# Performance work log

Hardware: AMD Instinct MI355X
Metric: run time of the kernel (lower is better)

Reference implementation:

```python
import jax, jax.numpy as jnp
import numpy as np

N_NODES = 33
EPS = 1e-5


def _tconv(x, w, b):
    # x: (B,T,N,Ci); w: (3,O,Ci,1,ks); b: (3,O). Gated temporal conv: relu(P*sigmoid(Q)+R)
    xt = jnp.transpose(x, (0, 3, 2, 1))  # (B,Ci,N,T)
    def c(i):
        y = jax.lax.conv_general_dilated(xt, w[i], (1, 1), 'VALID',
                                         dimension_numbers=('NCHW', 'OIHW', 'NCHW'))
        return y + b[i][None, :, None, None]
    P, Q, R = c(0), c(1), c(2)
    H = jax.nn.relu(P * jax.nn.sigmoid(Q) + R)
    return jnp.transpose(H, (0, 3, 2, 1))  # (B,T',N,O)


def _cheb(x, edge_index, Wk, bias):
    # ChebConv K=3, sym normalization, lambda_max=2 => L_hat = -D^{-1/2} A D^{-1/2} (diag cancels)
    src, tgt = edge_index[0], edge_index[1]
    w = jnp.ones((src.shape[0],), x.dtype)
    deg = jnp.zeros((N_NODES,), x.dtype).at[src].add(w)
    dinv = jnp.where(deg > 0, deg ** -0.5, 0.0)
    lap_w = -dinv[src] * w * dinv[tgt]

    def prop(z):  # z: (B,T,N,C); sparse matvec over edges, aggregate at target
        zg = z[:, :, src, :] * lap_w[None, None, :, None]
        return jnp.zeros_like(z).at[:, :, tgt, :].add(zg)

    Tx0 = x
    Tx1 = prop(Tx0)
    Tx2 = 2.0 * prop(Tx1) - Tx0
    out = (jnp.einsum('btnc,cd->btnd', Tx0, Wk[0])
           + jnp.einsum('btnc,cd->btnd', Tx1, Wk[1])
           + jnp.einsum('btnc,cd->btnd', Tx2, Wk[2]))
    return out + bias


def _bn(x, g, b):
    # BatchNorm2d(num_nodes): stats per node over (B,T,C); biased variance, train-mode stats
    mean = x.mean(axis=(0, 1, 3), keepdims=True)
    var = x.var(axis=(0, 1, 3), keepdims=True)
    return (x - mean) * jax.lax.rsqrt(var + EPS) * g[None, None, :, None] + b[None, None, :, None]


def _stconv(x, ei, tc1w, tc1b, cw, cb, tc2w, tc2b, bng, bnb):
    t = _tconv(x, tc1w, tc1b)
    t = jax.nn.relu(_cheb(t, ei, cw, cb))
    t = _tconv(t, tc2w, tc2b)
    return _bn(t, bng, bnb)


def setup_inputs() -> dict:
    key = jax.random.key(0)
    ks = jax.random.split(key, 24)
    s = 0.05
    inp = {
        'x': jax.random.normal(ks[0], (32, 512, 33, 3), jnp.float32),
        'edge_index': jax.random.randint(ks[1], (2, 64), 0, 33, jnp.int64) if jax.config.jax_enable_x64 else jax.random.randint(ks[1], (2, 64), 0, 33).astype(jnp.int32),
        # STConv 1 (in=3, hid=out=64)
        's1_tc1_w': jax.random.normal(ks[2], (3, 64, 3, 1, 3), jnp.float32) * s,
        's1_tc1_b': jax.random.normal(ks[3], (3, 64), jnp.float32) * s,
        's1_cheb_w': jax.random.normal(ks[4], (3, 64, 64), jnp.float32) * s,
        's1_cheb_b': jax.random.normal(ks[5], (64,), jnp.float32) * s,
        's1_tc2_w': jax.random.normal(ks[6], (3, 64, 64, 1, 3), jnp.float32) * s,
        's1_tc2_b': jax.random.normal(ks[7], (3, 64), jnp.float32) * s,
        's1_bn_g': jnp.ones((33,), jnp.float32),
        's1_bn_b': jnp.zeros((33,), jnp.float32),
        # STConv 2 (in=64, hid=out=64)
        's2_tc1_w': jax.random.normal(ks[8], (3, 64, 64, 1, 3), jnp.float32) * s,
        's2_tc1_b': jax.random.normal(ks[9], (3, 64), jnp.float32) * s,
        's2_cheb_w': jax.random.normal(ks[10], (3, 64, 64), jnp.float32) * s,
        's2_cheb_b': jax.random.normal(ks[11], (64,), jnp.float32) * s,
        's2_tc2_w': jax.random.normal(ks[12], (3, 64, 64, 1, 3), jnp.float32) * s,
        's2_tc2_b': jax.random.normal(ks[13], (3, 64), jnp.float32) * s,
        's2_bn_g': jnp.ones((33,), jnp.float32),
        's2_bn_b': jnp.zeros((33,), jnp.float32),
        # classifier: Linear(64*33 -> 256), Linear(256 -> 10)
        'fc1_w': jax.random.normal(ks[14], (64 * 33, 256), jnp.float32) * s,
        'fc1_b': jax.random.normal(ks[15], (256,), jnp.float32) * s,
        'fc2_w': jax.random.normal(ks[16], (256, 10), jnp.float32) * s,
        'fc2_b': jax.random.normal(ks[17], (10,), jnp.float32) * s,
    }
    return inp


def reference(x, edge_index,
              s1_tc1_w, s1_tc1_b, s1_cheb_w, s1_cheb_b, s1_tc2_w, s1_tc2_b, s1_bn_g, s1_bn_b,
              s2_tc1_w, s2_tc1_b, s2_cheb_w, s2_cheb_b, s2_tc2_w, s2_tc2_b, s2_bn_g, s2_bn_b,
              fc1_w, fc1_b, fc2_w, fc2_b):
    h = jax.nn.relu(_stconv(x, edge_index, s1_tc1_w, s1_tc1_b, s1_cheb_w, s1_cheb_b,
                            s1_tc2_w, s1_tc2_b, s1_bn_g, s1_bn_b))
    h = jax.nn.relu(_stconv(h, edge_index, s2_tc1_w, s2_tc1_b, s2_cheb_w, s2_cheb_b,
                            s2_tc2_w, s2_tc2_b, s2_bn_g, s2_bn_b))
    h = h.mean(axis=1)                      # (B, N, C) mean over time
    h = h.reshape(h.shape[0], -1)           # (B, N*C)
    h = jax.nn.relu(h @ fc1_w + fc1_b)      # dropout = identity (eval)
    return h @ fc2_w + fc2_b                # (B, num_classes)
```

## Files before the change

### kernel.cpp

```cpp
#include <hip/hip_runtime.h>
#include <math.h>

#define NN 33
#define NC 2112

typedef __attribute__((ext_vector_type(8))) short bfrag;
typedef __attribute__((ext_vector_type(4))) float f32x4;

#define OFF_LT   0
#define OFF_L2T  2244
#define OFF_UP1  4488
#define OFF_UP2  16776
#define OFF_WT0  29064
#define OFF_WT1  65928
#define OFF_WT2  102792
#define OFF_ST1  139656
#define OFF_ST2  139722
#define OFF_HB   139856
#define OFF_MEAN 148048
#define OFF_A    215632
#define A_ELEMS  34332672ull
#define SLAB     1077120ull

__device__ inline unsigned short f2bf(float x) {
  unsigned int u = __float_as_uint(x);
  unsigned int r = (u + 0x7fffu + ((u >> 16) & 1u)) >> 16;
  return (unsigned short)r;
}
__device__ inline float bf2f(unsigned short h) {
  return __uint_as_float(((unsigned int)h) << 16);
}

__global__ __launch_bounds__(256) void k_prep_lap(
    const int* __restrict__ ei, float* __restrict__ ws) {
  __shared__ float Lsm[1089];
  __shared__ float L2sm[1089];
  __shared__ float deg[NN];
  __shared__ float dinv[NN];
  int tid = threadIdx.x;
  for (int i = tid; i < 1089; i += 256) Lsm[i] = 0.f;
  if (tid < NN) deg[tid] = 0.f;
  __syncthreads();
  if (tid < 64) atomicAdd(&deg[ei[tid]], 1.f);
  __syncthreads();
  if (tid < NN) dinv[tid] = deg[tid] > 0.f ? rsqrtf(deg[tid]) : 0.f;
  __syncthreads();
  if (tid < 64) {
    int s = ei[tid], t = ei[64 + tid];
    atomicAdd(&Lsm[t * NN + s], -dinv[s] * dinv[t]);
  }
  __syncthreads();
  for (int i = tid; i < 1089; i += 256) {
    int r = i / NN, c = i % NN;
    float s = 0.f;
    for (int m = 0; m < NN; m++) s += Lsm[r * NN + m] * Lsm[m * NN + c];
    L2sm[i] = 2.f * s;
  }
  __syncthreads();
  for (int i = tid; i < 33 * 66; i += 256) {
    int m = i / 66, nn = i % 66;
    int n33 = nn < 33 ? nn : nn - 33;
    ws[OFF_LT + m * 68 + nn]  = Lsm[n33 * NN + m];
    ws[OFF_L2T + m * 68 + nn] = L2sm[n33 * NN + m];
  }
}

__global__ __launch_bounds__(256) void k_prep_w(
    const float* __restrict__ cw1, const float* __restrict__ cw2,
    const float* __restrict__ tw0, const float* __restrict__ tw1,
    const float* __restrict__ tw2, float* __restrict__ ws) {
  int u = blockIdx.x * 256 + threadIdx.x;
  if (u < 24576) {
    unsigned short* u1 = (unsigned short*)(ws + OFF_UP1);
    unsigned short* u2 = (unsigned short*)(ws + OFF_UP2);
    int j = u & 7;
    int nn = (u >> 3) & 15;
    int q = (u >> 7) & 3;
    int sp = (u >> 9) & 1;
    int blk = u >> 10;
    int nt = blk & 3;
    int ks = blk >> 2;
    int k = ks * 32 + q * 8 + j;
    int d = nt * 16 + nn;
    int s = k >> 6, cc = k & 63;
    float v1 = cw1[(s * 64 + cc) * 64 + d];
    float v2 = cw2[(s * 64 + cc) * 64 + d];
    if (s == 0) { v1 -= cw1[(128 + cc) * 64 + d]; v2 -= cw2[(128 + cc) * 64 + d]; }
    unsigned short h1 = f2bf(v1);
    u1[u] = sp ? f2bf(v1 - bf2f(h1)) : h1;
    unsigned short h2 = f2bf(v2);
    u2[u] = sp ? f2bf(v2 - bf2f(h2)) : h2;
  }
  {
    unsigned short* p0 = (unsigned short*)(ws + OFF_WT0);
    unsigned short* p1 = (unsigned short*)(ws + OFF_WT1);
    unsigned short* p2 = (unsigned short*)(ws + OFF_WT2);
    int j  = u & 7;
    int nn_ = (u >> 3) & 15;
    int q  = (u >> 7) & 3;
    int B  = u >> 9;
    int sp = B & 1;
    int B2 = B >> 1;
    int nt = B2 % 12;
    int dk = B2 / 12;
    int ks = dk & 1;
    int dt = dk >> 1;
    int o  = nt * 16 + nn_;
    int ci = ks * 32 + q * 8 + j;
    int src = (o * 64 + ci) * 3 + dt;
    float w0 = tw0[src], w1 = tw1[src], w2 = tw2[src];
    unsigned short h;
    h = f2bf(w0); p0[u] = sp ? f2bf(w0 - bf2f(h)) : h;
    h = f2bf(w1); p1[u] = sp ? f2bf(w1 - bf2f(h)) : h;
    h = f2bf(w2); p2[u] = sp ? f2bf(w2 - bf2f(h)) : h;
  }
}

__global__ __launch_bounds__(256) void k_tconv0(
    const float* __restrict__ x, const float* __restrict__ w,
    const float* __restrict__ bias, float* __restrict__ out,
    int b0, int total) {
  __shared__ float wsm[1728];
  __shared__ float bsm[192];
  int tid = threadIdx.x;
  for (int i = tid; i < 1728; i += 256) wsm[i] = w[i];
  if (tid < 192) bsm[tid] = bias[tid];
  __syncthreads();
  int idx = blockIdx.x * 256 + tid;
  if (idx >= total) return;
  int ch = idx & 63;
  int r = idx >> 6;
  int n = r % NN; r /= NN;
  int t = r % 510;
  int bc = r / 510;
  int b = b0 + bc;
  float aP = bsm[ch], aQ = bsm[64 + ch], aR = bsm[128 + ch];
  const float* xp = x + ((size_t)(b * 512 + t) * NN + n) * 3;
  #pragma unroll
  for (int dt = 0; dt < 3; dt++) {
    float x0 = xp[dt * 99 + 0], x1 = xp[dt * 99 + 1], x2 = xp[dt * 99 + 2];
    aP += x0 * wsm[(ch * 3 + 0) * 3 + dt] + x1 * wsm[(ch * 3 + 1) * 3 + dt] + x2 * wsm[(ch * 3 + 2) * 3 + dt];
    aQ += x0 * wsm[((64 + ch) * 3 + 0) * 3 + dt] + x1 * wsm[((64 + ch) * 3 + 1) * 3 + dt] + x2 * wsm[((64 + ch) * 3 + 2) * 3 + dt];
    aR += x0 * wsm[((128 + ch) * 3 + 0) * 3 + dt] + x1 * wsm[((128 + ch) * 3 + 1) * 3 + dt] + x2 * wsm[((128 + ch) * 3 + 2) * 3 + dt];
  }
  float sg = 1.f / (1.f + __expf(-aQ));
  out[(size_t)(bc * 510 + t) * NC + n * 64 + ch] = fmaxf(aP * sg + aR, 0.f);
}

__global__ __launch_bounds__(256, 4) void k_chebmm(
    const float* __restrict__ in, const unsigned short* __restrict__ Uf,
    const float* __restrict__ cbias, float* __restrict__ out,
    const float* __restrict__ ws, int totalRows) {
  __shared__ __attribute__((aligned(16))) unsigned short Zh[64 * 136];
  __shared__ __attribute__((aligned(16))) unsigned short Zl[64 * 136];

  int tid = threadIdx.x;
  int R0 = blockIdx.x * 64;
  int c = tid & 63;
  int g = __builtin_amdgcn_readfirstlane(tid >> 6);
  int Rg = R0 + g * 16;
  int btg = Rg / 33;
  int n0 = Rg - btg * 33;
  int wrap = 33 - n0;

  const float* lt  = ws + OFF_LT;
  const float* l2t = ws + OFF_L2T;
  const float* ipA = in + (size_t)btg * NC + c;
  const float* ipB = ipA + NC;
  float z1[16], z2[16];
  #pragma unroll
  for (int rr = 0; rr < 16; rr++) { z1[rr] = 0.f; z2[rr] = 0.f; }
  #pragma unroll 3
  for (int m = 0; m < NN; m++) {
    float hvA = ipA[m * 64];
    float hvB = ipB[m * 64];
    const float* ltm  = lt + m * 68 + n0;
    const float* l2tm = l2t + m * 68 + n0;
    #pragma unroll
    for (int rr = 0; rr < 16; rr++) {
      float hv = (rr < wrap) ? hvA : hvB;
      z1[rr] += ltm[rr] * hv;
      z2[rr] += l2tm[rr] * hv;
    }
  }
  #pragma unroll
  for (int rr = 0; rr < 16; rr++) {
    int r = g * 16 + rr;
    unsigned short zh1 = f2bf(z1[rr]);
    Zh[r * 136 + c] = zh1;
    Zl[r * 136 + c] = f2bf(z1[rr] - bf2f(zh1));
    unsigned short zh2 = f2bf(z2[rr]);
    Zh[r * 136 + 64 + c] = zh2;
    Zl[r * 136 + 64 + c] = f2bf(z2[rr] - bf2f(zh2));
  }

  int lane = tid & 63;
  int m15 = lane & 15, q = lane >> 4;
  f32x4 acc[4];
  #pragma unroll
  for (int nt = 0; nt < 4; nt++) acc[nt] = (f32x4){0.f, 0.f, 0.f, 0.f};

  const float* hrow = in + (size_t)(Rg + m15) * 64 + q * 8;
  float hv0[8], hv1[8];
  *(float4*)&hv0[0] = *(const float4*)(hrow);
  *(float4*)&hv0[4] = *(const float4*)(hrow + 4);
  *(float4*)&hv1[0] = *(const float4*)(hrow + 32);
  *(float4*)&hv1[4] = *(const float4*)(hrow + 36);

  bfrag uh[4], ul[4];
  #pragma unroll
  for (int nt = 0; nt < 4; nt++) {
    const unsigned short* bp = Uf + nt * 1024 + lane * 8;
    uh[nt] = *(const bfrag*)bp;
    ul[nt] = *(const bfrag*)(bp + 512);
  }

  #pragma unroll
  for (int ks = 0; ks < 6; ks++) {
    bfrag nh[4], nl[4];
    if (ks < 5) {
      #pragma unroll
      for (int nt = 0; nt < 4; nt++) {
        const unsigned short* bp = Uf + ((ks + 1) * 4 + nt) * 1024 + lane * 8;
        nh[nt] = *(const bfrag*)bp;
        nl[nt] = *(const bfrag*)(bp + 512);
      }
    }
    bfrag ah, al;
    if (ks < 2) {
      const float* hv = (ks == 0) ? hv0 : hv1;
      union { bfrag v; unsigned short s[8]; } Ahf, Alf;
      #pragma unroll
      for (int j = 0; j < 8; j++) {
        unsigned short hh = f2bf(hv[j]);
        Ahf.s[j] = hh;
        Alf.s[j] = f2bf(hv[j] - bf2f(hh));
      }
      ah = Ahf.v; al = Alf.v;
    } else {
      int aoff = (g * 16 + m15) * 136 + (ks - 2) * 32 + q * 8;
      ah = *(const bfrag*)(Zh + aoff);
      al = *(const bfrag*)(Zl + aoff);
    }
    #pragma unroll
    for (int nt = 0; nt < 4; nt++) {
      acc[nt] = __builtin_amdgcn_mfma_f32_16x16x32_bf16(ah, uh[nt], acc[nt], 0, 0, 0);
      acc[nt] = __builtin_amdgcn_mfma_f32_16x16x32_bf16(ah, ul[nt], acc[nt], 0, 0, 0);
      acc[nt] = __builtin_amdgcn_mfma_f32_16x16x32_bf16(al, uh[nt], acc[nt], 0, 0, 0);
    }
    #pragma unroll
    for (int nt = 0; nt < 4; nt++) { uh[nt] = nh[nt]; ul[nt] = nl[nt]; }
  }
  #pragma unroll
  for (int nt = 0; nt < 4; nt++) {
    int d = nt * 16 + m15;
    float bd = cbias[d];
    #pragma unroll
    for (int rr = 0; rr < 4; rr++) {
      int R = R0 + g * 16 + q * 4 + rr;
      if (R < totalRows)
        out[(size_t)R * 64 + d] = fmaxf(acc[nt][rr] + bd, 0.f);
    }
  }
}

__global__ __launch_bounds__(256, 4) void k_tconv(
    const float* __restrict__ in, int inStride, int Tin,
    const unsigned short* __restrict__ wsp, const float* __restrict__ bias,
    float* __restrict__ out, int outStride, int Tout,
    const float* __restrict__ bnSt, const float* __restrict__ bnG,
    const float* __restrict__ bnB, float bnCnt, float* __restrict__ statsOut) {
  __shared__ __attribute__((aligned(16))) unsigned short Ah[66 * 72];
  __shared__ __attribute__((aligned(16))) unsigned short Al[66 * 72];
  __shared__ float red[8];
  int tid = threadIdx.x;
  int ntt = (Tout + 63) >> 6;
  int tpb = NN * ntt;
  int bc = blockIdx.x / tpb, r = blockIdx.x % tpb;
  int n = r / ntt, tt = r % ntt;
  int t0 = tt << 6;
  const float* ip = in + (size_t)bc * inStride * NC + n * 64;

  float sc = 1.f, sh = 0.f;
  if (bnSt) {
    float mean = bnSt[n] / bnCnt;
    float var = bnSt[33 + n] / bnCnt - mean * mean;
    sc = rsqrtf(var + 1e-5f) * bnG[n];
    sh = bnB[n] - mean * sc;
  }
  for (int i = tid; i < 66 * 16; i += 256) {
    int row = i >> 4, c4 = i & 15;
    float4 v = make_float4(0.f, 0.f, 0.f, 0.f);
    if (t0 + row < Tin) v = *(const float4*)(ip + (size_t)(t0 + row) * NC + c4 * 4);
    if (bnSt) {
      v.x = fmaxf(v.x * sc + sh, 0.f);
      v.y = fmaxf(v.y * sc + sh, 0.f);
      v.z = fmaxf(v.z * sc + sh, 0.f);
      v.w = fmaxf(v.w * sc + sh, 0.f);
    }
    unsigned short h0 = f2bf(v.x), h1 = f2bf(v.y), h2 = f2bf(v.z), h3 = f2bf(v.w);
    unsigned short l0 = f2bf(v.x - bf2f(h0)), l1 = f2bf(v.y - bf2f(h1));
    unsigned short l2 = f2bf(v.z - bf2f(h2)), l3 = f2bf(v.w - bf2f(h3));
    uint2 ph, pl;
    ph.x = (unsigned)h0 | ((unsigned)h1 << 16); ph.y = (unsigned)h2 | ((unsigned)h3 << 16);
    pl.x = (unsigned)l0 | ((unsigned)l1 << 16); pl.y = (unsigned)l2 | ((unsigned)l3 << 16);
    *(uint2*)(Ah + row * 72 + c4 * 4) = ph;
    *(uint2*)(Al + row * 72 + c4 * 4) = pl;
  }
  __syncthreads();

  int lane = tid & 63;
  int wv = tid >> 6;
  int m15 = lane & 15, q = lane >> 4;

  f32x4 acc[4][3];
  #pragma unroll
  for (int mi = 0; mi < 4; mi++)
    #pragma unroll
    for (int j = 0; j < 3; j++) acc[mi][j] = (f32x4){0.f, 0.f, 0.f, 0.f};

  #pragma unroll
  for (int s = 0; s < 6; s++) {
    int dt = s >> 1, ks = s & 1;
    const unsigned short* wdt = wsp + (size_t)dt * 24576;
    bfrag bh[3], bl[3];
    #pragma unroll
    for (int j = 0; j < 3; j++) {
      int nt = wv + 4 * j;
      const unsigned short* bp = wdt + ((ks * 12 + nt) * 2) * 512 + lane * 8;
      bh[j] = *(const bfrag*)bp;
      bl[j] = *(const bfrag*)(bp + 512);
    }
    bfrag ah[4], al[4];
    #pragma unroll
    for (int mi = 0; mi < 4; mi++) {
      int row = mi * 16 + m15 + dt;
      int off = row * 72 + ks * 32 + q * 8;
      ah[mi] = *(const bfrag*)(Ah + off);
      al[mi] = *(const bfrag*)(Al + off);
    }
    #pragma unroll
    for (int j = 0; j < 3; j++)
      #pragma unroll
      for (int mi = 0; mi < 4; mi++) {
        acc[mi][j] = __builtin_amdgcn_mfma_f32_16x16x32_bf16(ah[mi], bh[j], acc[mi][j], 0, 0, 0);
        acc[mi][j] = __builtin_amdgcn_mfma_f32_16x16x32_bf16(ah[mi], bl[j], acc[mi][j], 0, 0, 0);
        acc[mi][j] = __builtin_amdgcn_mfma_f32_16x16x32_bf16(al[mi], bh[j], acc[mi][j], 0, 0, 0);
      }
  }

  float ssum = 0.f, sq = 0.f;
  int ch = wv * 16 + m15;
  float bP = bias[ch], bQ = bias[64 + ch], bR = bias[128 + ch];
  #pragma unroll
  for (int mi = 0; mi < 4; mi++) {
    #pragma unroll
    for (int rr = 0; rr < 4; rr++) {
      int t = t0 + mi * 16 + q * 4 + rr;
      float P = acc[mi][0][rr] + bP;
      float Q = acc[mi][1][rr] + bQ;
      float Rv = acc[mi][2][rr] + bR;
      float sg = 1.f / (1.f + __expf(-Q));
      float h = fmaxf(P * sg + Rv, 0.f);
      if (t < Tout) {
        out[(size_t)(bc * outStride + t) * NC + n * 64 + ch] = h;
        ssum += h; sq += h * h;
      }
    }
  }
  if (statsOut) {
    #pragma unroll
    for (int d = 32; d > 0; d >>= 1) {
      ssum += __shfl_down(ssum, d);
      sq += __shfl_down(sq, d);
    }
    if (lane == 0) { red[wv] = ssum; red[4 + wv] = sq; }
    __syncthreads();
    if (tid == 0) {
      atomicAdd(&statsOut[n], red[0] + red[1] + red[2] + red[3]);
      atomicAdd(&statsOut[33 + n], red[4] + red[5] + red[6] + red[7]);
    }
  }
}

__global__ __launch_bounds__(256) void k_bnmean(
    const float* __restrict__ A, int stride, int Tv,
    const float* __restrict__ st, const float* __restrict__ gg,
    const float* __restrict__ bb, float* __restrict__ mout) {
  int idx = blockIdx.x * 256 + threadIdx.x;
  int p = idx % NC, b = idx / NC;
  int n = p >> 6;
  float cnt = (float)(32 * Tv * 64);
  float mean = st[n] / cnt;
  float var = st[33 + n] / cnt - mean * mean;
  float sc = rsqrtf(var + 1e-5f) * gg[n];
  float sh = bb[n] - mean * sc;
  float acc = 0.f;
  const float* ap = A + (size_t)b * stride * NC + p;
  for (int t = 0; t < Tv; t += 4) {
    acc += fmaxf(ap[(size_t)t * NC] * sc + sh, 0.f)
         + fmaxf(ap[(size_t)(t + 1) * NC] * sc + sh, 0.f)
         + fmaxf(ap[(size_t)(t + 2) * NC] * sc + sh, 0.f)
         + fmaxf(ap[(size_t)(t + 3) * NC] * sc + sh, 0.f);
  }
  mout[idx] = acc / (float)Tv;
}

__global__ __launch_bounds__(256) void k_fc1(
    const float* __restrict__ meanb, const float* __restrict__ w1,
    float* __restrict__ hb) {
  int b = blockIdx.x >> 3, ks = blockIdx.x & 7;
  int d = threadIdx.x;
  const float* mp = meanb + b * NC + ks * 264;
  const float* wp = w1 + (size_t)(ks * 264) * 256 + d;
  float acc = 0.f;
  for (int k = 0; k < 264; k += 8) {
    #pragma unroll
    for (int u = 0; u < 8; u++)
      acc += mp[k + u] * wp[(size_t)(k + u) * 256];
  }
  atomicAdd(&hb[b * 256 + d], acc);
}

__global__ __launch_bounds__(256) void k_fc2(
    const float* __restrict__ hb, const float* __restrict__ b1,
    const float* __restrict__ w2, const float* __restrict__ b2,
    float* __restrict__ out) {
  __shared__ float h[256];
  int tid = threadIdx.x, b = blockIdx.x;
  h[tid] = fmaxf(hb[b * 256 + tid] + b1[tid], 0.f);
  __syncthreads();
  if (tid < 10) {
    float a = b2[tid];
    for (int k = 0; k < 256; k++) a += h[k] * w2[k * 10 + tid];
    out[b * 10 + tid] = a;
  }
}

extern "C" void kernel_launch(void* const* d_in, const int* in_sizes, int n_in,
                              void* d_out, int out_size, void* d_ws, size_t ws_size,
                              hipStream_t stream) {
  const float* x        = (const float*)d_in[0];
  const int*   ei       = (const int*)d_in[1];
  const float* s1_tc1_w = (const float*)d_in[2];
  const float* s1_tc1_b = (const float*)d_in[3];
  const float* s1_cheb_w= (const float*)d_in[4];
  const float* s1_cheb_b= (const float*)d_in[5];
  const float* s1_tc2_w = (const float*)d_in[6];
  const float* s1_tc2_b = (const float*)d_in[7];
  const float* s1_bn_g  = (const float*)d_in[8];
  const float* s1_bn_b  = (const float*)d_in[9];
  const float* s2_tc1_w = (const float*)d_in[10];
  const float* s2_tc1_b = (const float*)d_in[11];
  const float* s2_cheb_w= (const float*)d_in[12];
  const float* s2_cheb_b= (const float*)d_in[13];
  const float* s2_tc2_w = (const float*)d_in[14];
  const float* s2_tc2_b = (const float*)d_in[15];
  const float* s2_bn_g  = (const float*)d_in[16];
  const float* s2_bn_b  = (const float*)d_in[17];
  const float* fc1_w    = (const float*)d_in[18];
  const float* fc1_b    = (const float*)d_in[19];
  const float* fc2_w    = (const float*)d_in[20];
  const float* fc2_b    = (const float*)d_in[21];
  float* ws  = (float*)d_ws;
  float* out = (float*)d_out;

  int chunk = 32;
  while (chunk > 1 &&
         ((size_t)OFF_A + A_ELEMS + (size_t)chunk * SLAB * 2) * 4 > ws_size)
    chunk >>= 1;
  float* A  = ws + OFF_A;
  float* HS = A + A_ELEMS;
  float* CS = HS + (size_t)chunk * SLAB;

  hipMemsetAsync(ws + OFF_ST1, 0, (OFF_HB + 8192 - OFF_ST1) * sizeof(float), stream);
  k_prep_lap<<<1, 256, 0, stream>>>(ei, ws);
  k_prep_w<<<288, 256, 0, stream>>>(s1_cheb_w, s2_cheb_w,
                                    s1_tc2_w, s2_tc1_w, s2_tc2_w, ws);

  const unsigned short* wt0 = (const unsigned short*)(ws + OFF_WT0);
  const unsigned short* wt1 = (const unsigned short*)(ws + OFF_WT1);
  const unsigned short* wt2 = (const unsigned short*)(ws + OFF_WT2);
  const unsigned short* uf1 = (const unsigned short*)(ws + OFF_UP1);
  const unsigned short* uf2 = (const unsigned short*)(ws + OFF_UP2);

  int nchunks = 32 / chunk;
  int rowsC = chunk * 510 * NN;
  int nblkC = (rowsC + 63) / 64;
  float cnt1 = (float)(32 * 508 * 64);
  for (int ci = 0; ci < nchunks; ci++) {
    int b0 = ci * chunk;
    int total0 = chunk * 510 * NC;
    k_tconv0<<<(total0 + 255) / 256, 256, 0, stream>>>(x, s1_tc1_w, s1_tc1_b,
                                                       HS, b0, total0);
    k_chebmm<<<nblkC, 256, 0, stream>>>(HS, uf1, s1_cheb_b, CS, ws, rowsC);
    k_tconv<<<chunk * NN * 8, 256, 0, stream>>>(CS, 510, 510, wt0, s1_tc2_b,
                                                A + (size_t)b0 * 508 * NC, 508, 508,
                                                nullptr, nullptr, nullptr, 1.f,
                                                ws + OFF_ST1);
  }
  for (int ci = 0; ci < nchunks; ci++) {
    int b0 = ci * chunk;
    k_tconv<<<chunk * NN * 8, 256, 0, stream>>>(A + (size_t)b0 * 508 * NC, 508, 508,
                                                wt1, s2_tc1_b, HS, 510, 506,
                                                ws + OFF_ST1, s1_bn_g, s1_bn_b, cnt1,
                                                nullptr);
    k_chebmm<<<nblkC, 256, 0, stream>>>(HS, uf2, s2_cheb_b, CS, ws, rowsC);
    k_tconv<<<chunk * NN * 8, 256, 0, stream>>>(CS, 510, 506, wt2, s2_tc2_b,
                                                A + (size_t)b0 * 508 * NC, 508, 504,
                                                nullptr, nullptr, nullptr, 1.f,
                                                ws + OFF_ST2);
  }
  k_bnmean<<<(32 * NC) / 256, 256, 0, stream>>>(A, 508, 504, ws + OFF_ST2,
                                                s2_bn_g, s2_bn_b, ws + OFF_MEAN);
  k_fc1<<<256, 256, 0, stream>>>(ws + OFF_MEAN, fc1_w, ws + OFF_HB);
  k_fc2<<<32, 256, 0, stream>>>(ws + OFF_HB, fc1_b, fc2_w, fc2_b, out);
}
```

Measured before the change: 1.350 ms.

## Merge prep kernels, prefetch tconv weights, drop block reduction, shrink chunk size

Folds the Laplacian prep into the weight-prep launch as an extra block, which saves one kernel launch. In the temporal-conv kernel, the next step's weight fragments are loaded one step ahead (software prefetch) to hide global load latency, at the cost of more registers. The per-block shared-memory stats reduction is replaced by a per-wave atomicAdd, trading a barrier for four times as many atomics. The batch chunk size drops from 32 to 8 so intermediate slabs stay smaller and more cache-resident, but this adds more launches.

```diff
diff --git a/kernel.cpp b/kernel.cpp
--- a/kernel.cpp
+++ b/kernel.cpp
@@ -31,45 +31,45 @@
   return __uint_as_float(((unsigned int)h) << 16);
 }
 
-__global__ __launch_bounds__(256) void k_prep_lap(
-    const int* __restrict__ ei, float* __restrict__ ws) {
-  __shared__ float Lsm[1089];
-  __shared__ float L2sm[1089];
-  __shared__ float deg[NN];
-  __shared__ float dinv[NN];
-  int tid = threadIdx.x;
-  for (int i = tid; i < 1089; i += 256) Lsm[i] = 0.f;
-  if (tid < NN) deg[tid] = 0.f;
-  __syncthreads();
-  if (tid < 64) atomicAdd(&deg[ei[tid]], 1.f);
-  __syncthreads();
-  if (tid < NN) dinv[tid] = deg[tid] > 0.f ? rsqrtf(deg[tid]) : 0.f;
-  __syncthreads();
-  if (tid < 64) {
-    int s = ei[tid], t = ei[64 + tid];
-    atomicAdd(&Lsm[t * NN + s], -dinv[s] * dinv[t]);
-  }
-  __syncthreads();
-  for (int i = tid; i < 1089; i += 256) {
-    int r = i / NN, c = i % NN;
-    float s = 0.f;
-    for (int m = 0; m < NN; m++) s += Lsm[r * NN + m] * Lsm[m * NN + c];
-    L2sm[i] = 2.f * s;
-  }
-  __syncthreads();
-  for (int i = tid; i < 33 * 66; i += 256) {
-    int m = i / 66, nn = i % 66;
-    int n33 = nn < 33 ? nn : nn - 33;
-    ws[OFF_LT + m * 68 + nn]  = Lsm[n33 * NN + m];
-    ws[OFF_L2T + m * 68 + nn] = L2sm[n33 * NN + m];
-  }
-}
-
-__global__ __launch_bounds__(256) void k_prep_w(
+__global__ __launch_bounds__(256) void k_prep(
+    const int* __restrict__ ei,
     const float* __restrict__ cw1, const float* __restrict__ cw2,
     const float* __restrict__ tw0, const float* __restrict__ tw1,
     const float* __restrict__ tw2, float* __restrict__ ws) {
-  int u = blockIdx.x * 256 + threadIdx.x;
+  int tid = threadIdx.x;
+  if (blockIdx.x == 288) {
+    __shared__ float Lsm[1089];
+    __shared__ float L2sm[1089];
+    __shared__ float deg[NN];
+    __shared__ float dinv[NN];
+    for (int i = tid; i < 1089; i += 256) Lsm[i] = 0.f;
+    if (tid < NN) deg[tid] = 0.f;
+    __syncthreads();
+    if (tid < 64) atomicAdd(&deg[ei[tid]], 1.f);
+    __syncthreads();
+    if (tid < NN) dinv[tid] = deg[tid] > 0.f ? rsqrtf(deg[tid]) : 0.f;
+    __syncthreads();
+    if (tid < 64) {
+      int s = ei[tid], t = ei[64 + tid];
+      atomicAdd(&Lsm[t * NN + s], -dinv[s] * dinv[t]);
+    }
+    __syncthreads();
+    for (int i = tid; i < 1089; i += 256) {
+      int r = i / NN, c = i % NN;
+      float s = 0.f;
+      for (int m = 0; m < NN; m++) s += Lsm[r * NN + m] * Lsm[m * NN + c];
+      L2sm[i] = 2.f * s;
+    }
+    __syncthreads();
+    for (int i = tid; i < 33 * 66; i += 256) {
+      int m = i / 66, nn = i % 66;
+      int n33 = nn < 33 ? nn : nn - 33;
+      ws[OFF_LT + m * 68 + nn]  = Lsm[n33 * NN + m];
+      ws[OFF_L2T + m * 68 + nn] = L2sm[n33 * NN + m];
+    }
+    return;
+  }
+  int u = blockIdx.x * 256 + tid;
   if (u < 24576) {
     unsigned short* u1 = (unsigned short*)(ws + OFF_UP1);
     unsigned short* u2 = (unsigned short*)(ws + OFF_UP2);
@@ -272,7 +272,6 @@
     const float* __restrict__ bnB, float bnCnt, float* __restrict__ statsOut) {
   __shared__ __attribute__((aligned(16))) unsigned short Ah[66 * 72];
   __shared__ __attribute__((aligned(16))) unsigned short Al[66 * 72];
-  __shared__ float red[8];
   int tid = threadIdx.x;
   int ntt = (Tout + 63) >> 6;
   int tpb = NN * ntt;
@@ -319,17 +318,29 @@
     #pragma unroll
     for (int j = 0; j < 3; j++) acc[mi][j] = (f32x4){0.f, 0.f, 0.f, 0.f};
 
+  bfrag bh[3], bl[3];
+  #pragma unroll
+  for (int j = 0; j < 3; j++) {
+    int nt = wv + 4 * j;
+    const unsigned short* bp = wsp + ((0 * 12 + nt) * 2) * 512 + lane * 8;
+    bh[j] = *(const bfrag*)bp;
+    bl[j] = *(const bfrag*)(bp + 512);
+  }
+
   #pragma unroll
   for (int s = 0; s < 6; s++) {
     int dt = s >> 1, ks = s & 1;
-    const unsigned short* wdt = wsp + (size_t)dt * 24576;
-    bfrag bh[3], bl[3];
-    #pragma unroll
-    for (int j = 0; j < 3; j++) {
-      int nt = wv + 4 * j;
-      const unsigned short* bp = wdt + ((ks * 12 + nt) * 2) * 512 + lane * 8;
-      bh[j] = *(const bfrag*)bp;
-      bl[j] = *(const bfrag*)(bp + 512);
+    bfrag nh[3], nl[3];
+    if (s < 5) {
+      int dt1 = (s + 1) >> 1, ks1 = (s + 1) & 1;
+      const unsigned short* wdt1 = wsp + (size_t)dt1 * 24576;
+      #pragma unroll
+      for (int j = 0; j < 3; j++) {
+        int nt = wv + 4 * j;
+        const unsigned short* bp = wdt1 + ((ks1 * 12 + nt) * 2) * 512 + lane * 8;
+        nh[j] = *(const bfrag*)bp;
+        nl[j] = *(const bfrag*)(bp + 512);
+      }
     }
     bfrag ah[4], al[4];
     #pragma unroll
@@ -347,6 +358,8 @@
         acc[mi][j] = __builtin_amdgcn_mfma_f32_16x16x32_bf16(ah[mi], bl[j], acc[mi][j], 0, 0, 0);
         acc[mi][j] = __builtin_amdgcn_mfma_f32_16x16x32_bf16(al[mi], bh[j], acc[mi][j], 0, 0, 0);
       }
+    #pragma unroll
+    for (int j = 0; j < 3; j++) { bh[j] = nh[j]; bl[j] = nl[j]; }
   }
 
   float ssum = 0.f, sq = 0.f;
@@ -374,11 +387,9 @@
       ssum += __shfl_down(ssum, d);
       sq += __shfl_down(sq, d);
     }
-    if (lane == 0) { red[wv] = ssum; red[4 + wv] = sq; }
-    __syncthreads();
-    if (tid == 0) {
-      atomicAdd(&statsOut[n], red[0] + red[1] + red[2] + red[3]);
-      atomicAdd(&statsOut[33 + n], red[4] + red[5] + red[6] + red[7]);
+    if (lane == 0) {
+      atomicAdd(&statsOut[n], ssum);
+      atomicAdd(&statsOut[33 + n], sq);
     }
   }
 }
@@ -465,7 +476,7 @@
   float* ws  = (float*)d_ws;
   float* out = (float*)d_out;
 
-  int chunk = 32;
+  int chunk = 8;
   while (chunk > 1 &&
          ((size_t)OFF_A + A_ELEMS + (size_t)chunk * SLAB * 2) * 4 > ws_size)
     chunk >>= 1;
@@ -474,9 +485,8 @@
   float* CS = HS + (size_t)chunk * SLAB;
 
   hipMemsetAsync(ws + OFF_ST1, 0, (OFF_HB + 8192 - OFF_ST1) * sizeof(float), stream);
-  k_prep_lap<<<1, 256, 0, stream>>>(ei, ws);
-  k_prep_w<<<288, 256, 0, stream>>>(s1_cheb_w, s2_cheb_w,
-                                    s1_tc2_w, s2_tc1_w, s2_tc2_w, ws);
+  k_prep<<<289, 256, 0, stream>>>(ei, s1_cheb_w, s2_cheb_w,
+                                  s1_tc2_w, s2_tc1_w, s2_tc2_w, ws);
 
   const unsigned short* wt0 = (const unsigned short*)(ws + OFF_WT0);
   const unsigned short* wt1 = (const unsigned short*)(ws + OFF_WT1);
```

After: 1.774 ms. +31.4%, slower.
